# Kernel tuning notes

Measured on AMD Instinct MI355X. Metric: run time of the kernel, lower is better.

The kernel has to match this reference:

```python
import jax, jax.numpy as jnp
import numpy as np

B, S, D, H = 32, 2048, 1024, 1024

def setup_inputs() -> dict:
    key = jax.random.key(0)
    k1, k2, k3, k4, k5 = jax.random.split(key, 5)
    return {
        "query": jax.random.normal(k1, (B, D), dtype=jnp.float32),
        "values": jax.random.normal(k2, (B, S, D), dtype=jnp.float32),
        "W1": jax.random.normal(k3, (D, H), dtype=jnp.float32) / np.sqrt(D),
        "W2": jax.random.normal(k4, (D, H), dtype=jnp.float32) / np.sqrt(D),
        "v": jax.random.uniform(k5, (H,), dtype=jnp.float32),
    }

def reference(query, values, W1, W2, v):
    # query: [B, D], values: [B, S, D]
    query_proj = query @ W2                              # [B, H]
    keys_proj = jnp.einsum('bsd,dh->bsh', values, W1)     # [B, S, H]
    energy = jnp.tanh(query_proj[:, None, :] + keys_proj) # [B, S, H]
    scores = jnp.einsum('bsh,h->bs', energy, v)           # [B, S]
    attention_weights = jax.nn.softmax(scores, axis=-1)   # [B, S]
    context = jnp.einsum('bs,bsd->bd', attention_weights, values)  # [B, D]
    return context, attention_weights
```

## Files before the change

kernel.cpp:

```cpp
#include <hip/hip_runtime.h>
#include <hip/hip_fp16.h>


typedef _Float16 v8h  __attribute__((ext_vector_type(8)));
typedef float    v4f  __attribute__((ext_vector_type(4)));

#define B_DIM 32
#define S_DIM 2048
#define D_DIM 1024
#define H_DIM 1024

#define WS_V16    0u
#define WS_W1T    134217728u
#define WS_QP     (WS_W1T + 2097152u)
#define WS_SCORES (WS_QP + 131072u)

__device__ __forceinline__ void gl_lds16(const _Float16* g, _Float16* l) {
    __builtin_amdgcn_global_load_lds(
        (const __attribute__((address_space(1))) void*)g,
        (__attribute__((address_space(3))) void*)l, 16, 0, 0);
}

__global__ void k_prep(const float* __restrict__ values, _Float16* __restrict__ v16,
                       const float* __restrict__ W1, _Float16* __restrict__ w1t,
                       const float* __restrict__ query, const float* __restrict__ W2,
                       float* __restrict__ qp, float* __restrict__ scores) {
    __shared__ float smem[64 * 65];
    int bid = blockIdx.x, tid = threadIdx.x;
    if (bid >= 544) {
        size_t i = ((size_t)(bid - 544) * 256 + tid) * 8;
        v4f f0 = __builtin_nontemporal_load((const v4f*)(values + i));
        v4f f1 = __builtin_nontemporal_load((const v4f*)(values + i + 4));
        v8h hv;
        hv[0] = (_Float16)f0[0]; hv[1] = (_Float16)f0[1];
        hv[2] = (_Float16)f0[2]; hv[3] = (_Float16)f0[3];
        hv[4] = (_Float16)f1[0]; hv[5] = (_Float16)f1[1];
        hv[6] = (_Float16)f1[2]; hv[7] = (_Float16)f1[3];
        *(v8h*)(v16 + i) = hv;
    } else if (bid < 256) {
        int b = bid >> 3, hc = bid & 7;
        #pragma unroll
        for (int i = 0; i < 4; ++i)
            smem[i * 256 + tid] = query[b * D_DIM + i * 256 + tid];
        __syncthreads();
        int hh = tid & 127, half = tid >> 7;
        int h = hc * 128 + hh;
        const float* w2p = W2 + (size_t)(half * 512) * H_DIM + h;
        float acc = 0.f;
        #pragma unroll 8
        for (int d = 0; d < 512; ++d)
            acc += smem[half * 512 + d] * w2p[(size_t)d * H_DIM];
        smem[1024 + tid] = acc;
        __syncthreads();
        if (tid < 128)
            qp[b * H_DIM + hc * 128 + tid] = smem[1024 + tid] + smem[1024 + 128 + tid];
    } else if (bid < 512) {
        int j = bid - 256;
        int h0 = (j & 15) * 64, d0 = (j >> 4) * 64;
        #pragma unroll
        for (int i = 0; i < 16; ++i) {
            int idx = i * 256 + tid;
            int dd = idx >> 6, hh = idx & 63;
            smem[dd * 65 + hh] = W1[(size_t)(d0 + dd) * H_DIM + h0 + hh];
        }
        __syncthreads();
        #pragma unroll
        for (int i = 0; i < 16; ++i) {
            int idx = i * 256 + tid;
            int hh = idx >> 6, dd = idx & 63;
            w1t[(size_t)(h0 + hh) * D_DIM + d0 + dd] = (_Float16)smem[dd * 65 + hh];
        }
    } else {
        int j = bid - 512;
        size_t o = (size_t)j * 2048 + tid * 8;
        *(v4f*)(scores + o)     = (v4f){0.f, 0.f, 0.f, 0.f};
        *(v4f*)(scores + o + 4) = (v4f){0.f, 0.f, 0.f, 0.f};
    }
}


template<bool PF>
__device__ __forceinline__ void gemm_step(
        const _Float16* CA, const _Float16* CB,
        _Float16* NA, _Float16* NB,
        const _Float16* a16, const _Float16* bw, int k1,
        int wm, int wn, int quad, int l15, int wid, int srow, int kg,
        v4f acc[8][4]) {
    #pragma unroll
    for (int kk = 0; kk < 2; ++kk) {
        v8h bf[4];
        #pragma unroll
        for (int j = 0; j < 4; ++j) {
            int row = wn * 64 + j * 16 + l15;
            int ph  = (kk * 4 + quad) ^ (row & 7);
            bf[j] = *(const v8h*)(&CB[row * 64 + ph * 8]);
        }
        #pragma unroll
        for (int mh = 0; mh < 2; ++mh) {
            v8h af[4];
            #pragma unroll
            for (int i = 0; i < 4; ++i) {
                int row = wm * 128 + mh * 64 + i * 16 + l15;
                int ph  = (kk * 4 + quad) ^ (row & 7);
                af[i] = *(const v8h*)(&CA[row * 64 + ph * 8]);
            }
            if (PF && kk == 0) {
                #pragma unroll
                for (int i = 0; i < 4; ++i) {
                    int brow = i * 64 + wid * 8;
                    int row  = brow + srow;
                    int kgs  = kg ^ (row & 7);
                    if (mh == 0)
                        gl_lds16(a16 + (size_t)row * D_DIM + k1 + kgs * 8,
                                 &NA[brow * 64]);
                    else
                        gl_lds16(bw + (size_t)row * D_DIM + k1 + kgs * 8,
                                 &NB[brow * 64]);
                }
            }
            __builtin_amdgcn_s_barrier();
            asm volatile("s_waitcnt lgkmcnt(0)" ::: "memory");
            __builtin_amdgcn_sched_barrier(0);
            __builtin_amdgcn_s_setprio(1);
            #pragma unroll
            for (int i = 0; i < 4; ++i)
                #pragma unroll
                for (int j = 0; j < 4; ++j)
                    acc[mh * 4 + i][j] = __builtin_amdgcn_mfma_f32_16x16x32_f16(
                        af[i], bf[j], acc[mh * 4 + i][j], 0, 0, 0);
            __builtin_amdgcn_s_setprio(0);
        }
    }
    if (PF) asm volatile("s_waitcnt vmcnt(0)" ::: "memory");
    __builtin_amdgcn_s_barrier();
}

__global__ __launch_bounds__(512, 2) void k_scores(
        const _Float16* __restrict__ v16, const _Float16* __restrict__ w1t,
        const float* __restrict__ qp, const float* __restrict__ v,
        float* __restrict__ scores) {
    __shared__ _Float16 As[2][256 * 64];
    __shared__ _Float16 Bs[2][256 * 64];

    int tid = threadIdx.x;
    int wid = tid >> 6, lane = tid & 63;
    int quad = lane >> 4, l15 = lane & 15;
    int wm = wid >> 2, wn = wid & 3;

    int bid = blockIdx.x;
    int idx = (bid & 7) * 128 + (bid >> 3);
    int np  = idx & 3;
    int mtb = idx >> 2;
    int b   = mtb >> 3;
    int m0  = (mtb & 7) * 256;
    int n0  = np * 256;

    int srow = lane >> 3;
    int kg   = lane & 7;
    const _Float16* a16 = v16 + ((size_t)b * S_DIM + m0) * D_DIM;
    const _Float16* bw  = w1t + (size_t)n0 * D_DIM;

    v4f acc[8][4];
    #pragma unroll
    for (int i = 0; i < 8; ++i)
        #pragma unroll
        for (int j = 0; j < 4; ++j) acc[i][j] = (v4f){0.f, 0.f, 0.f, 0.f};

    #pragma unroll
    for (int i = 0; i < 4; ++i) {
        int brow = i * 64 + wid * 8;
        int row  = brow + srow;
        int kgs  = kg ^ (row & 7);
        gl_lds16(a16 + (size_t)row * D_DIM + kgs * 8, &As[0][brow * 64]);
        gl_lds16(bw  + (size_t)row * D_DIM + kgs * 8, &Bs[0][brow * 64]);
    }
    asm volatile("s_waitcnt vmcnt(0)" ::: "memory");
    __builtin_amdgcn_s_barrier();

    for (int t = 0; t < 15; ++t) {
        int cur = t & 1;
        gemm_step<true>(As[cur], Bs[cur], As[cur ^ 1], Bs[cur ^ 1],
                        a16, bw, (t + 1) * 64,
                        wm, wn, quad, l15, wid, srow, kg, acc);
    }
    gemm_step<false>(As[1], Bs[1], As[0], Bs[0], a16, bw, 0,
                     wm, wn, quad, l15, wid, srow, kg, acc);

    float qpv[4], vv[4];
    #pragma unroll
    for (int nt = 0; nt < 4; ++nt) {
        int ng = n0 + wn * 64 + nt * 16 + l15;
        qpv[nt] = qp[b * H_DIM + ng];
        vv[nt]  = v[ng];
    }

    float* s_scores = (float*)&As[0][0];
    if (tid < 256) s_scores[tid] = 0.f;
    __syncthreads();

    #pragma unroll
    for (int mt = 0; mt < 8; ++mt) {
        #pragma unroll
        for (int r = 0; r < 4; ++r) {
            float s = 0.f;
            #pragma unroll
            for (int nt = 0; nt < 4; ++nt) {
                float x = acc[mt][nt][r] + qpv[nt];
                float e = __expf(2.f * x);
                s += (1.f - 2.f / (e + 1.f)) * vv[nt];
            }
            s += __shfl_xor(s, 1);
            s += __shfl_xor(s, 2);
            s += __shfl_xor(s, 4);
            s += __shfl_xor(s, 8);
            if (l15 == 0)
                atomicAdd(&s_scores[wm * 128 + mt * 16 + quad * 4 + r], s);
        }
    }
    __syncthreads();
    if (tid < 256) atomicAdd(&scores[(size_t)b * S_DIM + m0 + tid], s_scores[tid]);
}

__global__ __launch_bounds__(1024) void k_finish(
        const float* __restrict__ scores, const float* __restrict__ values,
        float* __restrict__ wout, float* __restrict__ ctx) {
    __shared__ float s_w[2048];
    __shared__ int   s_idx[2048];
    __shared__ float red[16];
    __shared__ float s_bcast;
    __shared__ int   s_cnt;

    int b = blockIdx.x, tid = threadIdx.x;
    int lane = tid & 63, wid = tid >> 6;

    float s0 = scores[b * S_DIM + tid];
    float s1 = scores[b * S_DIM + 1024 + tid];

    float m = fmaxf(s0, s1);
    #pragma unroll
    for (int off = 1; off <= 32; off <<= 1) m = fmaxf(m, __shfl_xor(m, off));
    if (lane == 0) red[wid] = m;
    if (tid == 0) s_cnt = 0;
    __syncthreads();
    if (tid == 0) {
        float mm = red[0];
        #pragma unroll
        for (int i = 1; i < 16; ++i) mm = fmaxf(mm, red[i]);
        s_bcast = mm;
    }
    __syncthreads();
    float rowmax = s_bcast;

    float e0 = __expf(s0 - rowmax);
    float e1 = __expf(s1 - rowmax);
    float sum = e0 + e1;
    #pragma unroll
    for (int off = 1; off <= 32; off <<= 1) sum += __shfl_xor(sum, off);
    if (lane == 0) red[wid] = sum;
    __syncthreads();
    if (tid == 0) {
        float ss = red[0];
        #pragma unroll
        for (int i = 1; i < 16; ++i) ss += red[i];
        s_bcast = 1.f / ss;
    }
    __syncthreads();
    float inv = s_bcast;

    float w0 = e0 * inv, w1 = e1 * inv;
    wout[b * S_DIM + tid]        = w0;
    wout[b * S_DIM + 1024 + tid] = w1;
    s_w[tid]        = w0;
    s_w[tid + 1024] = w1;

    if (w0 > 1e-7f) { int p = atomicAdd(&s_cnt, 1); s_idx[p] = tid; }
    if (w1 > 1e-7f) { int p = atomicAdd(&s_cnt, 1); s_idx[p] = tid + 1024; }
    __syncthreads();
    int cnt = s_cnt;

    float acc = 0.f;
    const float* vb = values + (size_t)b * S_DIM * D_DIM + tid;
    for (int i = 0; i < cnt; ++i) {
        int s = s_idx[i];
        acc += s_w[s] * vb[(size_t)s * D_DIM];
    }
    ctx[b * D_DIM + tid] = acc;
}

extern "C" void kernel_launch(void* const* d_in, const int* in_sizes, int n_in,
                              void* d_out, int out_size, void* d_ws, size_t ws_size,
                              hipStream_t stream) {
    const float* query  = (const float*)d_in[0];
    const float* values = (const float*)d_in[1];
    const float* W1     = (const float*)d_in[2];
    const float* W2     = (const float*)d_in[3];
    const float* v      = (const float*)d_in[4];

    char* ws = (char*)d_ws;
    _Float16* v16 = (_Float16*)(ws + WS_V16);
    _Float16* w1t = (_Float16*)(ws + WS_W1T);
    float* qp     = (float*)(ws + WS_QP);
    float* scores = (float*)(ws + WS_SCORES);

    float* ctx  = (float*)d_out;
    float* wout = (float*)d_out + 32768;

    k_prep<<<dim3(33312), 256, 0, stream>>>(values, v16, W1, w1t, query, W2, qp, scores);
    k_scores<<<dim3(1024), 512, 0, stream>>>(v16, w1t, qp, v, scores);
    k_finish<<<dim3(32), 1024, 0, stream>>>(scores, values, wout, ctx);
}
```

Measured before the change: 556.9 us.

## Software-pipeline LDS fragment reads with MFMA using register double buffering

Restructures the GEMM main loop so LDS fragment reads for the next MFMA group are issued before the current group executes. Two register sets per operand and partial lgkmcnt waits replace the full lgkmcnt(0) wait and the per-half-step barrier. The next tile's first fragments are read right after the single per-step barrier, so they overlap the last MFMA group. This uses more registers and relies on exact lgkmcnt counting, which risks spills at 2 blocks/CU or ordering hazards.

Measured after the change: 558.3 us. About the same (+0.3%).

```diff
diff --git a/kernel.cpp b/kernel.cpp
--- a/kernel.cpp
+++ b/kernel.cpp
@@ -79,61 +79,43 @@
 }
 
 
-template<bool PF>
-__device__ __forceinline__ void gemm_step(
-        const _Float16* CA, const _Float16* CB,
-        _Float16* NA, _Float16* NB,
-        const _Float16* a16, const _Float16* bw, int k1,
-        int wm, int wn, int quad, int l15, int wid, int srow, int kg,
-        v4f acc[8][4]) {
-    #pragma unroll
-    for (int kk = 0; kk < 2; ++kk) {
-        v8h bf[4];
-        #pragma unroll
-        for (int j = 0; j < 4; ++j) {
-            int row = wn * 64 + j * 16 + l15;
-            int ph  = (kk * 4 + quad) ^ (row & 7);
-            bf[j] = *(const v8h*)(&CB[row * 64 + ph * 8]);
-        }
-        #pragma unroll
-        for (int mh = 0; mh < 2; ++mh) {
-            v8h af[4];
-            #pragma unroll
-            for (int i = 0; i < 4; ++i) {
-                int row = wm * 128 + mh * 64 + i * 16 + l15;
-                int ph  = (kk * 4 + quad) ^ (row & 7);
-                af[i] = *(const v8h*)(&CA[row * 64 + ph * 8]);
-            }
-            if (PF && kk == 0) {
-                #pragma unroll
-                for (int i = 0; i < 4; ++i) {
-                    int brow = i * 64 + wid * 8;
-                    int row  = brow + srow;
-                    int kgs  = kg ^ (row & 7);
-                    if (mh == 0)
-                        gl_lds16(a16 + (size_t)row * D_DIM + k1 + kgs * 8,
-                                 &NA[brow * 64]);
-                    else
-                        gl_lds16(bw + (size_t)row * D_DIM + k1 + kgs * 8,
-                                 &NB[brow * 64]);
-                }
-            }
-            __builtin_amdgcn_s_barrier();
-            asm volatile("s_waitcnt lgkmcnt(0)" ::: "memory");
-            __builtin_amdgcn_sched_barrier(0);
-            __builtin_amdgcn_s_setprio(1);
-            #pragma unroll
-            for (int i = 0; i < 4; ++i)
-                #pragma unroll
-                for (int j = 0; j < 4; ++j)
-                    acc[mh * 4 + i][j] = __builtin_amdgcn_mfma_f32_16x16x32_f16(
-                        af[i], bf[j], acc[mh * 4 + i][j], 0, 0, 0);
-            __builtin_amdgcn_s_setprio(0);
-        }
-    }
-    if (PF) asm volatile("s_waitcnt vmcnt(0)" ::: "memory");
-    __builtin_amdgcn_s_barrier();
-}
+#define SB __builtin_amdgcn_sched_barrier(0)
+
+#define READ_AF(dst, CA, mh, kk)                                           \
+    _Pragma("unroll")                                                      \
+    for (int i_ = 0; i_ < 4; ++i_) {                                       \
+        int row_ = wm * 128 + (mh) * 64 + i_ * 16 + l15;                   \
+        int ph_  = ((kk) * 4 + quad) ^ (row_ & 7);                         \
+        dst[i_] = *(const v8h*)(&(CA)[row_ * 64 + ph_ * 8]);               \
+    }
+
+#define READ_BF(dst, CB, kk)                                               \
+    _Pragma("unroll")                                                      \
+    for (int j_ = 0; j_ < 4; ++j_) {                                       \
+        int row_ = wn * 64 + j_ * 16 + l15;                                \
+        int ph_  = ((kk) * 4 + quad) ^ (row_ & 7);                         \
+        dst[j_] = *(const v8h*)(&(CB)[row_ * 64 + ph_ * 8]);               \
+    }
+
+#define MFMA16(af, bf, mh)                                                 \
+    __builtin_amdgcn_s_setprio(1);                                         \
+    _Pragma("unroll")                                                      \
+    for (int i_ = 0; i_ < 4; ++i_)                                         \
+        _Pragma("unroll")                                                  \
+        for (int j_ = 0; j_ < 4; ++j_)                                     \
+            acc[(mh) * 4 + i_][j_] = __builtin_amdgcn_mfma_f32_16x16x32_f16( \
+                af[i_], bf[j_], acc[(mh) * 4 + i_][j_], 0, 0, 0);          \
+    __builtin_amdgcn_s_setprio(0);
+
+#define STAGE(dstbuf, src, koff)                                           \
+    _Pragma("unroll")                                                      \
+    for (int i_ = 0; i_ < 4; ++i_) {                                       \
+        int brow_ = i_ * 64 + wid * 8;                                     \
+        int row_  = brow_ + srow;                                          \
+        int kgs_  = kg ^ (row_ & 7);                                       \
+        gl_lds16((src) + (size_t)row_ * D_DIM + (koff) + kgs_ * 8,         \
+                 &(dstbuf)[brow_ * 64]);                                   \
+    }
 
 __global__ __launch_bounds__(512, 2) void k_scores(
         const _Float16* __restrict__ v16, const _Float16* __restrict__ w1t,
@@ -166,25 +148,49 @@
         #pragma unroll
         for (int j = 0; j < 4; ++j) acc[i][j] = (v4f){0.f, 0.f, 0.f, 0.f};
 
-    #pragma unroll
-    for (int i = 0; i < 4; ++i) {
-        int brow = i * 64 + wid * 8;
-        int row  = brow + srow;
-        int kgs  = kg ^ (row & 7);
-        gl_lds16(a16 + (size_t)row * D_DIM + kgs * 8, &As[0][brow * 64]);
-        gl_lds16(bw  + (size_t)row * D_DIM + kgs * 8, &Bs[0][brow * 64]);
-    }
+    v8h af_a[4], af_b[4], bf_a[4], bf_b[4];
+
+    STAGE(As[0], a16, 0);
+    STAGE(Bs[0], bw, 0);
     asm volatile("s_waitcnt vmcnt(0)" ::: "memory");
     __builtin_amdgcn_s_barrier();
-
-    for (int t = 0; t < 15; ++t) {
-        int cur = t & 1;
-        gemm_step<true>(As[cur], Bs[cur], As[cur ^ 1], Bs[cur ^ 1],
-                        a16, bw, (t + 1) * 64,
-                        wm, wn, quad, l15, wid, srow, kg, acc);
-    }
-    gemm_step<false>(As[1], Bs[1], As[0], Bs[0], a16, bw, 0,
-                     wm, wn, quad, l15, wid, srow, kg, acc);
+    READ_AF(af_a, As[0], 0, 0);
+    READ_BF(bf_a, Bs[0], 0);
+
+    #pragma unroll 1
+    for (int t = 0; t < 16; ++t) {
+        const _Float16* cA = As[t & 1];
+        const _Float16* cB = Bs[t & 1];
+        _Float16* nA = As[(t + 1) & 1];
+        _Float16* nB = Bs[(t + 1) & 1];
+        int k1 = ((t + 1) & 15) * 64;
+        bool pf = (t < 15);
+
+        if (pf) STAGE(nA, a16, k1);
+        READ_AF(af_b, cA, 1, 0);
+        SB; asm volatile("s_waitcnt lgkmcnt(4)" ::: "memory"); SB;
+        MFMA16(af_a, bf_a, 0); SB;
+
+        if (pf) STAGE(nB, bw, k1);
+        READ_AF(af_a, cA, 0, 1);
+        READ_BF(bf_b, cB, 1);
+        SB; asm volatile("s_waitcnt lgkmcnt(8)" ::: "memory"); SB;
+        MFMA16(af_b, bf_a, 1); SB;
+
+        READ_AF(af_b, cA, 1, 1);
+        SB; asm volatile("s_waitcnt lgkmcnt(4)" ::: "memory"); SB;
+        MFMA16(af_a, bf_b, 0); SB;
+
+        asm volatile("s_waitcnt vmcnt(0) lgkmcnt(0)" ::: "memory");
+        __builtin_amdgcn_s_barrier();
+
+        if (pf) {
+            READ_AF(af_a, nA, 0, 0);
+            READ_BF(bf_a, nB, 0);
+        }
+        SB;
+        MFMA16(af_b, bf_b, 1); SB;
+    }
 
     float qpv[4], vv[4];
     #pragma unroll
```
